# Kernel tuning notes

Measured on AMD Instinct MI355X. Metric: run time of the kernel, lower is better.

## Reference

```python
import jax, jax.numpy as jnp
import numpy as np

B, T, C, L = 512, 512, 96, 64
BLANK = C - 1          # keras ctc_batch_cost uses last class as blank
EPS = 1e-7             # keras.backend.epsilon()
NEG = -1e30            # log-space 'zero'


def setup_inputs() -> dict:
    key = jax.random.key(0)
    k1, k2, k3 = jax.random.split(key, 3)
    # y_pred is expected to be a softmax output (probabilities over classes)
    y_pred = jax.nn.softmax(jax.random.normal(k1, (B, T, C), dtype=jnp.float32), axis=-1)
    # labels exclude the blank class (values in [0, C-2])
    y_true = jax.random.randint(k2, (B, L), 0, C - 1).astype(jnp.int32)
    label_length = jax.random.randint(k3, (B, 1), 16, L + 1).astype(jnp.int32)
    # forward slices y_pred[:, 2:, :] -> effective time length T-2 = 510
    input_length = jnp.full((B, 1), T - 2, dtype=jnp.int32)
    return {"y_true": y_true, "y_pred": y_pred,
            "input_length": input_length, "label_length": label_length}


def _ctc_forward(logprobs, labels, input_len, label_len):
    """CTC negative log-likelihood via the forward (alpha) DP in log space.
    logprobs: [B, Tp, C] log-probabilities; labels: [B, L] int;
    input_len, label_len: [B] int. Returns [B] loss."""
    Bn, Tp, Cn = logprobs.shape
    Ln = labels.shape[1]
    S = 2 * Ln + 1
    s = jnp.arange(S)
    lab_idx = jnp.clip(s // 2, 0, Ln - 1)
    # extended label sequence: blank, l1, blank, l2, ..., blank  -> [B, S]
    ext = jnp.where(s[None, :] % 2 == 1, labels[:, lab_idx], BLANK)
    ext2 = jnp.concatenate([jnp.full((Bn, 2), -1, ext.dtype), ext[:, :-2]], axis=1)
    allow_skip = (ext != BLANK) & (ext != ext2)  # [B, S]

    # gather per-timestep log-probs of extended labels: [Tp, B, S]
    lp_t = jnp.transpose(logprobs, (1, 0, 2))
    lp_ext = jnp.take_along_axis(lp_t, jnp.broadcast_to(ext[None], (Tp, Bn, S)), axis=2)

    # t = 0 init: only s=0 (blank) and s=1 (first label) reachable
    alpha0 = jnp.where(s[None, :] < 2, lp_ext[0], NEG)  # [B, S]

    def step(alpha, xs):
        lp, t = xs
        a1 = jnp.concatenate([jnp.full((Bn, 1), NEG, alpha.dtype), alpha[:, :-1]], axis=1)
        a2 = jnp.concatenate([jnp.full((Bn, 2), NEG, alpha.dtype), alpha[:, :-2]], axis=1)
        a2 = jnp.where(allow_skip, a2, NEG)
        new = jnp.logaddexp(jnp.logaddexp(alpha, a1), a2) + lp
        # freeze alpha once past each sequence's input length
        alpha = jnp.where((t < input_len)[:, None], new, alpha)
        return alpha, None

    ts = jnp.arange(1, Tp)
    alpha, _ = jax.lax.scan(step, alpha0, (lp_ext[1:], ts))

    s_last = 2 * label_len  # index of final blank in extended sequence
    a_last = jnp.take_along_axis(alpha, s_last[:, None], axis=1)[:, 0]
    a_prev = jnp.take_along_axis(alpha, (s_last - 1)[:, None], axis=1)[:, 0]
    return -jnp.logaddexp(a_last, a_prev)


def reference(y_true, y_pred, input_length, label_length):
    # CTCLayer.call: crop first two timesteps, then keras ctc_batch_cost
    y_pred = y_pred[:, 2:, :]
    # keras: logits = log(probs + eps); tf.nn.ctc_loss then log-softmaxes internally
    logits = jnp.log(y_pred + EPS)
    logprobs = jax.nn.log_softmax(logits, axis=-1)
    loss = _ctc_forward(logprobs, y_true,
                        input_length.reshape(-1).astype(jnp.int32),
                        label_length.reshape(-1).astype(jnp.int32))
    return loss[:, None]  # [B, 1], matching ctc_batch_cost's expand_dims
```

## Files before the change

kernel.cpp:

```cpp
#include <hip/hip_runtime.h>


constexpr int   T_    = 512;
constexpr int   C_    = 96;
constexpr int   L_    = 64;
constexpr int   TP_   = 510;
constexpr float EPS_  = 1e-7f;
constexpr float LN2_  = 0.69314718055994530942f;
constexpr float LSE1_ = 1.3849806e-5f;

typedef float f8 __attribute__((ext_vector_type(8)));
typedef float f2 __attribute__((ext_vector_type(2)));

__device__ __forceinline__ float flog2(float x) {
#if __has_builtin(__builtin_amdgcn_logf)
  return __builtin_amdgcn_logf(x);
#else
  return log2f(x);
#endif
}
__device__ __forceinline__ float fexp2(float x) {
#if __has_builtin(__builtin_amdgcn_exp2f)
  return __builtin_amdgcn_exp2f(x);
#else
  return exp2f(x);
#endif
}
__device__ __forceinline__ float fldexp(float x, int n) {
#if __has_builtin(__builtin_amdgcn_ldexpf)
  return __builtin_amdgcn_ldexpf(x, n);
#else
  return __builtin_ldexpf(x, n);
#endif
}

template<int CTRL, int RM, int BM, bool BC>
__device__ __forceinline__ float dppf(float old_, float src) {
  return __int_as_float(__builtin_amdgcn_update_dpp(
      __float_as_int(old_), __float_as_int(src), CTRL, RM, BM, BC));
}
template<int CTRL, int RM, int BM, bool BC>
__device__ __forceinline__ int dppi(int old_, int src) {
  return __builtin_amdgcn_update_dpp(old_, src, CTRL, RM, BM, BC);
}

__device__ __forceinline__ float lae2(float x, float y) {
  float m = fmaxf(x, y);
  return m + flog2(1.f + fexp2(-fabsf(x - y)));
}

#define LOADG(PL, PB, T0) {                                         \
  const float* _bl = colL + (size_t)(T0) * C_;                      \
  const float* _bb = colB + (size_t)(T0) * C_;                      \
  PL.s0=_bl[0*C_]; PB.s0=_bb[0*C_]; PL.s1=_bl[1*C_]; PB.s1=_bb[1*C_];\
  PL.s2=_bl[2*C_]; PB.s2=_bb[2*C_]; PL.s3=_bl[3*C_]; PB.s3=_bb[3*C_];\
  PL.s4=_bl[4*C_]; PB.s4=_bb[4*C_]; PL.s5=_bl[5*C_]; PB.s5=_bb[5*C_];\
  PL.s6=_bl[6*C_]; PB.s6=_bb[6*C_]; PL.s7=_bl[7*C_]; PB.s7=_bb[7*C_]; }

#define LD1C(PL, PB, T0, J) {                                       \
  int _t = (T0) + (J); _t = _t < TP_ ? _t : TP_ - 1;                \
  PL.s##J = colL[(size_t)_t * C_]; PB.s##J = colB[(size_t)_t * C_]; }
#define LOADGC(PL, PB, T0) \
  LD1C(PL,PB,T0,0) LD1C(PL,PB,T0,1) LD1C(PL,PB,T0,2) LD1C(PL,PB,T0,3) \
  LD1C(PL,PB,T0,4) LD1C(PL,PB,T0,5) LD1C(PL,PB,T0,6) LD1C(PL,PB,T0,7)

#define A8(PL, PB) { stepF(PL.s0,PB.s0); stepF(PL.s1,PB.s1);        \
  stepF(PL.s2,PB.s2); stepF(PL.s3,PB.s3); stepF(PL.s4,PB.s4);       \
  stepF(PL.s5,PB.s5); stepF(PL.s6,PB.s6); stepF(PL.s7,PB.s7); }

#define B8(PL, PB) { stepS(PL.s0,PB.s0); stepS(PL.s1,PB.s1);        \
  stepS(PL.s2,PB.s2); stepS(PL.s3,PB.s3); renormS();                \
  stepS(PL.s4,PB.s4); stepS(PL.s5,PB.s5); stepS(PL.s6,PB.s6);       \
  stepS(PL.s7,PB.s7); renormS(); }

#define TAIL1(PL, PB, J, OFF) \
  if ((tb + (OFF) + (J)) < tmax) stepF(PL.s##J, PB.s##J);
#define TAIL8(PL, PB, OFF) \
  TAIL1(PL,PB,0,OFF) TAIL1(PL,PB,1,OFF) TAIL1(PL,PB,2,OFF) TAIL1(PL,PB,3,OFF) \
  TAIL1(PL,PB,4,OFF) TAIL1(PL,PB,5,OFF) TAIL1(PL,PB,6,OFF) TAIL1(PL,PB,7,OFF)

__global__ __launch_bounds__(64, 1) void ctc_fwd(
    const int* __restrict__ y_true, const float* __restrict__ y_pred,
    const int* __restrict__ input_len, const int* __restrict__ label_len,
    float* __restrict__ out)
{
  const int b = blockIdx.x;
  const int l = threadIdx.x;

  const float* __restrict__ rp = y_pred + (size_t)b * T_ * C_ + 2 * C_;
  const int  lab     = y_true[b * L_ + l];
  const int  labPrev = __shfl_up(lab, 1);
  const float skipM  = (l >= 1 && lab != labPrev) ? 1.f : 0.f;
  const int  ilen    = input_len[b];
  const int  llen    = label_len[b];
  const int  tmax    = ilen < TP_ ? ilen : TP_;

  const float* __restrict__ colL = rp + lab;
  const float* __restrict__ colB = rp + (C_ - 1);

  f2    m;
  float mX = 0.f;
  int   e = 0, d = 0;
  m.x = (l == 0) ? (colB[0] + EPS_) : 0.f;
  m.y = (l == 0) ? (colL[0] + EPS_) : 0.f;

  f8 pl0, pl1, pl2, pl3, pb0, pb1, pb2, pb3;
  LOADG(pl0, pb0, 1);  LOADG(pl1, pb1, 9);
  LOADG(pl2, pb2, 17); LOADG(pl3, pb3, 25);

  auto runDP = [&](auto has128) {
    constexpr bool H128 = decltype(has128)::value;

    auto stepF = [&](float pl, float pb) {
      float plE = pl + EPS_, pbE = pb + EPS_;
      int   en  = dppi<0x138, 0xf, 0xf, false>(0, e);
      float m1  = dppf<0x138, 0xf, 0xf, false>(0.f, m.y);
      int   dd  = en - e;  dd = dd < 120 ? dd : 120;
      float a1  = fldexp(m1, dd);
      float nE  = (m.x + a1) * pbE;
      float nO  = fmaf(a1, skipM, m.y + m.x) * plE;
      float nX = 0.f, mx;
      if constexpr (H128) { nX = (mX + m.y) * pbE; mx = fmaxf(fmaxf(nE, nO), nX); }
      else                { mx = fmaxf(nE, nO); }
      int  kb = __float_as_int(mx) >> 23;
      int  ks = 127 - kb;
      bool z  = (mx == 0.f);
      e  = z ? en : (e + kb - 127);
      m.x = fldexp(nE, ks);
      m.y = fldexp(nO, ks);
      if constexpr (H128) mX = fldexp(nX, ks);
    };

    auto stepS = [&](float pl, float pb) {
      f2 p2;  p2.x = pb + EPS_;  p2.y = pl + EPS_;
      float m1 = dppf<0x138, 0xf, 0xf, false>(0.f, m.y);
      float a1 = fldexp(m1, d);
      float t  = fmaf(a1, skipM, m.x);
      if constexpr (H128) mX = (mX + m.y) * p2.x;
      f2 ad;  ad.x = a1;  ad.y = t;
      m = (m + ad) * p2;
    };

    auto renormS = [&]() {
      float mx = fmaxf(m.x, m.y);
      if constexpr (H128) mx = fmaxf(mx, mX);
      int kb = __float_as_int(mx) >> 23;
      int ks = 127 - kb;
      e += kb - 127;
      m.x = fldexp(m.x, ks);
      m.y = fldexp(m.y, ks);
      if constexpr (H128) mX = fldexp(mX, ks);
      int en = dppi<0x138, 0xf, 0xf, false>(0, e);
      int dd = en - e;  d = dd < 120 ? dd : 120;
    };

    int tb = 1;
#pragma unroll 1
    for (; tb < 65 && tb + 64 <= tmax; tb += 32) {
      A8(pl0, pb0); LOADG(pl0, pb0, tb + 32);
      A8(pl1, pb1); LOADG(pl1, pb1, tb + 40);
      A8(pl2, pb2); LOADG(pl2, pb2, tb + 48);
      A8(pl3, pb3); LOADG(pl3, pb3, tb + 56);
    }
    renormS();
#pragma unroll 1
    for (; tb + 64 <= tmax; tb += 32) {
      B8(pl0, pb0); LOADG(pl0, pb0, tb + 32);
      B8(pl1, pb1); LOADG(pl1, pb1, tb + 40);
      B8(pl2, pb2); LOADG(pl2, pb2, tb + 48);
      B8(pl3, pb3); LOADG(pl3, pb3, tb + 56);
    }
#pragma unroll 1
    for (; tb + 32 <= tmax; tb += 32) {
      A8(pl0, pb0); LOADGC(pl0, pb0, tb + 32);
      A8(pl1, pb1); LOADGC(pl1, pb1, tb + 40);
      A8(pl2, pb2); LOADGC(pl2, pb2, tb + 48);
      A8(pl3, pb3); LOADGC(pl3, pb3, tb + 56);
    }
    TAIL8(pl0, pb0, 0); TAIL8(pl1, pb1, 8);
    TAIL8(pl2, pb2, 16); TAIL8(pl3, pb3, 24);
  };

  if (llen >= 64) runDP(std::integral_constant<bool, true>{});
  else            runDP(std::integral_constant<bool, false>{});

  float ef  = (float)e;
  float lgE = flog2(m.x) + ef;
  float lgO = flog2(m.y) + ef;
  float aL;
  if (llen >= 64) { float lgX = flog2(mX) + ef; aL = __shfl(lgX, 63); }
  else            { aL = __shfl(lgE, llen); }
  float aP = __shfl(lgO, llen - 1);
  if (l == 0)
    out[b] = -LN2_ * (lae2(aL, aP) - (float)tmax * LSE1_);
}

extern "C" void kernel_launch(void* const* d_in, const int* in_sizes, int n_in,
                              void* d_out, int out_size, void* d_ws, size_t ws_size,
                              hipStream_t stream) {
  const int*   y_true = (const int*)d_in[0];
  const float* y_pred = (const float*)d_in[1];
  const int*   ilen   = (const int*)d_in[2];
  const int*   llen   = (const int*)d_in[3];
  float*       outp   = (float*)d_out;
  const int    B      = out_size;
  hipLaunchKernelGGL(ctc_fwd, dim3(B), dim3(64), 0, stream,
                     y_true, y_pred, ilen, llen, outp);
}
```

Before: 31.88 us.

## Split CTC kernel into producer wave loading to LDS and consumer DP wave

```diff
diff --git a/kernel.cpp b/kernel.cpp
--- a/kernel.cpp
+++ b/kernel.cpp
@@ -49,43 +49,76 @@
   return m + flog2(1.f + fexp2(-fabsf(x - y)));
 }
 
-#define LOADG(PL, PB, T0) {                                         \
-  const float* _bl = colL + (size_t)(T0) * C_;                      \
-  const float* _bb = colB + (size_t)(T0) * C_;                      \
-  PL.s0=_bl[0*C_]; PB.s0=_bb[0*C_]; PL.s1=_bl[1*C_]; PB.s1=_bb[1*C_];\
-  PL.s2=_bl[2*C_]; PB.s2=_bb[2*C_]; PL.s3=_bl[3*C_]; PB.s3=_bb[3*C_];\
-  PL.s4=_bl[4*C_]; PB.s4=_bb[4*C_]; PL.s5=_bl[5*C_]; PB.s5=_bb[5*C_];\
-  PL.s6=_bl[6*C_]; PB.s6=_bb[6*C_]; PL.s7=_bl[7*C_]; PB.s7=_bb[7*C_]; }
-
-#define LD1C(PL, PB, T0, J) {                                       \
-  int _t = (T0) + (J); _t = _t < TP_ ? _t : TP_ - 1;                \
-  PL.s##J = colL[(size_t)_t * C_]; PB.s##J = colB[(size_t)_t * C_]; }
-#define LOADGC(PL, PB, T0) \
-  LD1C(PL,PB,T0,0) LD1C(PL,PB,T0,1) LD1C(PL,PB,T0,2) LD1C(PL,PB,T0,3) \
-  LD1C(PL,PB,T0,4) LD1C(PL,PB,T0,5) LD1C(PL,PB,T0,6) LD1C(PL,PB,T0,7)
-
-#define A8(PL, PB) { stepF(PL.s0,PB.s0); stepF(PL.s1,PB.s1);        \
-  stepF(PL.s2,PB.s2); stepF(PL.s3,PB.s3); stepF(PL.s4,PB.s4);       \
-  stepF(PL.s5,PB.s5); stepF(PL.s6,PB.s6); stepF(PL.s7,PB.s7); }
-
-#define B8(PL, PB) { stepS(PL.s0,PB.s0); stepS(PL.s1,PB.s1);        \
-  stepS(PL.s2,PB.s2); stepS(PL.s3,PB.s3); renormS();                \
-  stepS(PL.s4,PB.s4); stepS(PL.s5,PB.s5); stepS(PL.s6,PB.s6);       \
-  stepS(PL.s7,PB.s7); renormS(); }
-
-#define TAIL1(PL, PB, J, OFF) \
-  if ((tb + (OFF) + (J)) < tmax) stepF(PL.s##J, PB.s##J);
-#define TAIL8(PL, PB, OFF) \
-  TAIL1(PL,PB,0,OFF) TAIL1(PL,PB,1,OFF) TAIL1(PL,PB,2,OFF) TAIL1(PL,PB,3,OFF) \
-  TAIL1(PL,PB,4,OFF) TAIL1(PL,PB,5,OFF) TAIL1(PL,PB,6,OFF) TAIL1(PL,PB,7,OFF)
-
-__global__ __launch_bounds__(64, 1) void ctc_fwd(
+#define PG8(R, TB) { \
+  R.s0 = gl((TB)+0); R.s1 = gl((TB)+1); R.s2 = gl((TB)+2); R.s3 = gl((TB)+3); \
+  R.s4 = gl((TB)+4); R.s5 = gl((TB)+5); R.s6 = gl((TB)+6); R.s7 = gl((TB)+7); }
+
+#define PLOADB(S, TB) { \
+  PG8(S##0, (TB)+0);  PG8(S##1, (TB)+8);  PG8(S##2, (TB)+16); PG8(S##3, (TB)+24); \
+  PG8(S##4, (TB)+32); PG8(S##5, (TB)+40); PG8(S##6, (TB)+48); PG8(S##7, (TB)+56); \
+  q##S = glb((TB) + l); }
+
+#define PW8(R, PH, TI) { \
+  plb[PH][(TI)+0][l] = R.s0; plb[PH][(TI)+1][l] = R.s1; \
+  plb[PH][(TI)+2][l] = R.s2; plb[PH][(TI)+3][l] = R.s3; \
+  plb[PH][(TI)+4][l] = R.s4; plb[PH][(TI)+5][l] = R.s5; \
+  plb[PH][(TI)+6][l] = R.s6; plb[PH][(TI)+7][l] = R.s7; }
+
+#define PWRITEB(S, PH) { \
+  PW8(S##0, PH, 0)  PW8(S##1, PH, 8)  PW8(S##2, PH, 16) PW8(S##3, PH, 24) \
+  PW8(S##4, PH, 32) PW8(S##5, PH, 40) PW8(S##6, PH, 48) PW8(S##7, PH, 56) \
+  pbb[PH][l] = q##S; }
+
+#define DSR8(PH, J, PL, PB) { \
+  PL.s0 = plb[PH][(J)*8+0][l]; PB.s0 = pbb[PH][(J)*8+0]; \
+  PL.s1 = plb[PH][(J)*8+1][l]; PB.s1 = pbb[PH][(J)*8+1]; \
+  PL.s2 = plb[PH][(J)*8+2][l]; PB.s2 = pbb[PH][(J)*8+2]; \
+  PL.s3 = plb[PH][(J)*8+3][l]; PB.s3 = pbb[PH][(J)*8+3]; \
+  PL.s4 = plb[PH][(J)*8+4][l]; PB.s4 = pbb[PH][(J)*8+4]; \
+  PL.s5 = plb[PH][(J)*8+5][l]; PB.s5 = pbb[PH][(J)*8+5]; \
+  PL.s6 = plb[PH][(J)*8+6][l]; PB.s6 = pbb[PH][(J)*8+6]; \
+  PL.s7 = plb[PH][(J)*8+7][l]; PB.s7 = pbb[PH][(J)*8+7]; }
+
+#define ST8(PL, PB) { renormS(); \
+  stepS(PL.s0,PB.s0); stepS(PL.s1,PB.s1); stepS(PL.s2,PB.s2); stepS(PL.s3,PB.s3); \
+  renormS(); \
+  stepS(PL.s4,PB.s4); stepS(PL.s5,PB.s5); stepS(PL.s6,PB.s6); stepS(PL.s7,PB.s7); }
+
+#define GD8(T0, PL, PB) { \
+  if ((T0)+0 < tmax) stepF(PL.s0,PB.s0); \
+  if ((T0)+1 < tmax) stepF(PL.s1,PB.s1); \
+  if ((T0)+2 < tmax) stepF(PL.s2,PB.s2); \
+  if ((T0)+3 < tmax) stepF(PL.s3,PB.s3); \
+  if ((T0)+4 < tmax) stepF(PL.s4,PB.s4); \
+  if ((T0)+5 < tmax) stepF(PL.s5,PB.s5); \
+  if ((T0)+6 < tmax) stepF(PL.s6,PB.s6); \
+  if ((T0)+7 < tmax) stepF(PL.s7,PB.s7); }
+
+#define COMPG(G, PL, PB) { const int _t0 = 1 + 8*(G); \
+  if ((G) >= 8 && (_t0 + 7) < tmax) ST8(PL, PB) else GD8(_t0, PL, PB) }
+
+#define CONSUME(PH, GB) { \
+  DSR8(PH, 0, plA, pbA); \
+  DSR8(PH, 1, plB, pbB); COMPG((GB)+0, plA, pbA); \
+  DSR8(PH, 2, plA, pbA); COMPG((GB)+1, plB, pbB); \
+  DSR8(PH, 3, plB, pbB); COMPG((GB)+2, plA, pbA); \
+  DSR8(PH, 4, plA, pbA); COMPG((GB)+3, plB, pbB); \
+  DSR8(PH, 5, plB, pbB); COMPG((GB)+4, plA, pbA); \
+  DSR8(PH, 6, plA, pbA); COMPG((GB)+5, plB, pbB); \
+  DSR8(PH, 7, plB, pbB); COMPG((GB)+6, plA, pbA); \
+                         COMPG((GB)+7, plB, pbB); }
+
+__global__ __launch_bounds__(128, 1) void ctc_fwd(
     const int* __restrict__ y_true, const float* __restrict__ y_pred,
     const int* __restrict__ input_len, const int* __restrict__ label_len,
     float* __restrict__ out)
 {
-  const int b = blockIdx.x;
-  const int l = threadIdx.x;
+  __shared__ float plb[2][64][64];
+  __shared__ float pbb[2][64];
+  const int tid = threadIdx.x;
+  const int wid = tid >> 6;
+  const int l   = tid & 63;
+  const int b   = blockIdx.x;
 
   const float* __restrict__ rp = y_pred + (size_t)b * T_ * C_ + 2 * C_;
   const int  lab     = y_true[b * L_ + l];
@@ -98,101 +131,101 @@
   const float* __restrict__ colL = rp + lab;
   const float* __restrict__ colB = rp + (C_ - 1);
 
-  f2    m;
+  auto gl  = [&](int t) -> float { int tc = t < TP_ ? t : TP_ - 1; return colL[(size_t)tc * C_]; };
+  auto glb = [&](int t) -> float { int tc = t < TP_ ? t : TP_ - 1; return colB[(size_t)tc * C_]; };
+
+  f2    mm;
   float mX = 0.f;
   int   e = 0, d = 0;
-  m.x = (l == 0) ? (colB[0] + EPS_) : 0.f;
-  m.y = (l == 0) ? (colL[0] + EPS_) : 0.f;
-
-  f8 pl0, pl1, pl2, pl3, pb0, pb1, pb2, pb3;
-  LOADG(pl0, pb0, 1);  LOADG(pl1, pb1, 9);
-  LOADG(pl2, pb2, 17); LOADG(pl3, pb3, 25);
-
-  auto runDP = [&](auto has128) {
-    constexpr bool H128 = decltype(has128)::value;
+  mm.x = (wid == 0 && l == 0) ? (colB[0] + EPS_) : 0.f;
+  mm.y = (wid == 0 && l == 0) ? (colL[0] + EPS_) : 0.f;
+
+  auto run = [&](auto hasC) {
+    constexpr bool H128 = decltype(hasC)::value;
 
     auto stepF = [&](float pl, float pb) {
       float plE = pl + EPS_, pbE = pb + EPS_;
       int   en  = dppi<0x138, 0xf, 0xf, false>(0, e);
-      float m1  = dppf<0x138, 0xf, 0xf, false>(0.f, m.y);
+      float m1  = dppf<0x138, 0xf, 0xf, false>(0.f, mm.y);
       int   dd  = en - e;  dd = dd < 120 ? dd : 120;
       float a1  = fldexp(m1, dd);
-      float nE  = (m.x + a1) * pbE;
-      float nO  = fmaf(a1, skipM, m.y + m.x) * plE;
+      float nE  = (mm.x + a1) * pbE;
+      float nO  = fmaf(a1, skipM, mm.y + mm.x) * plE;
       float nX = 0.f, mx;
-      if constexpr (H128) { nX = (mX + m.y) * pbE; mx = fmaxf(fmaxf(nE, nO), nX); }
+      if constexpr (H128) { nX = (mX + mm.y) * pbE; mx = fmaxf(fmaxf(nE, nO), nX); }
       else                { mx = fmaxf(nE, nO); }
       int  kb = __float_as_int(mx) >> 23;
       int  ks = 127 - kb;
       bool z  = (mx == 0.f);
       e  = z ? en : (e + kb - 127);
-      m.x = fldexp(nE, ks);
-      m.y = fldexp(nO, ks);
+      mm.x = fldexp(nE, ks);
+      mm.y = fldexp(nO, ks);
       if constexpr (H128) mX = fldexp(nX, ks);
     };
 
     auto stepS = [&](float pl, float pb) {
       f2 p2;  p2.x = pb + EPS_;  p2.y = pl + EPS_;
-      float m1 = dppf<0x138, 0xf, 0xf, false>(0.f, m.y);
+      float m1 = dppf<0x138, 0xf, 0xf, false>(0.f, mm.y);
       float a1 = fldexp(m1, d);
-      float t  = fmaf(a1, skipM, m.x);
-      if constexpr (H128) mX = (mX + m.y) * p2.x;
+      float t  = fmaf(a1, skipM, mm.x);
+      if constexpr (H128) mX = (mX + mm.y) * p2.x;
       f2 ad;  ad.x = a1;  ad.y = t;
-      m = (m + ad) * p2;
+      mm = (mm + ad) * p2;
     };
 
     auto renormS = [&]() {
-      float mx = fmaxf(m.x, m.y);
+      float mx = fmaxf(mm.x, mm.y);
       if constexpr (H128) mx = fmaxf(mx, mX);
       int kb = __float_as_int(mx) >> 23;
       int ks = 127 - kb;
       e += kb - 127;
-      m.x = fldexp(m.x, ks);
-      m.y = fldexp(m.y, ks);
+      mm.x = fldexp(mm.x, ks);
+      mm.y = fldexp(mm.y, ks);
       if constexpr (H128) mX = fldexp(mX, ks);
       int en = dppi<0x138, 0xf, 0xf, false>(0, e);
       int dd = en - e;  d = dd < 120 ? dd : 120;
     };
 
-    int tb = 1;
+    f8 A0,A1,A2,A3,A4,A5,A6,A7, C0,C1,C2,C3,C4,C5,C6,C7;
+    float qA, qC;
+    f8 plA, plB, pbA, pbB;
+
+    if (wid == 1) { PLOADB(A, 1) PLOADB(C, 65) }
+
 #pragma unroll 1
-    for (; tb < 65 && tb + 64 <= tmax; tb += 32) {
-      A8(pl0, pb0); LOADG(pl0, pb0, tb + 32);
-      A8(pl1, pb1); LOADG(pl1, pb1, tb + 40);
-      A8(pl2, pb2); LOADG(pl2, pb2, tb + 48);
-      A8(pl3, pb3); LOADG(pl3, pb3, tb + 56);
+    for (int mp = 0; mp < 8; ++mp) {
+      if (wid == 1) {
+        if (mp & 1) {
+          if (mp < 7) PLOADB(A, 1 + 64 * (mp + 1))
+          PWRITEB(C, 1)
+        } else {
+          if (mp >= 2) PLOADB(C, 1 + 64 * (mp + 1))
+          PWRITEB(A, 0)
+        }
+      } else if (mp >= 1) {
+        const int ph = (mp - 1) & 1;
+        const int gb = (mp - 1) * 8;
+        CONSUME(ph, gb)
+      }
+      __syncthreads();
     }
-    renormS();
-#pragma unroll 1
-    for (; tb + 64 <= tmax; tb += 32) {
-      B8(pl0, pb0); LOADG(pl0, pb0, tb + 32);
-      B8(pl1, pb1); LOADG(pl1, pb1, tb + 40);
-      B8(pl2, pb2); LOADG(pl2, pb2, tb + 48);
-      B8(pl3, pb3); LOADG(pl3, pb3, tb + 56);
-    }
-#pragma unroll 1
-    for (; tb + 32 <= tmax; tb += 32) {
-      A8(pl0, pb0); LOADGC(pl0, pb0, tb + 32);
-      A8(pl1, pb1); LOADGC(pl1, pb1, tb + 40);
-      A8(pl2, pb2); LOADGC(pl2, pb2, tb + 48);
-      A8(pl3, pb3); LOADGC(pl3, pb3, tb + 56);
-    }
-    TAIL8(pl0, pb0, 0); TAIL8(pl1, pb1, 8);
-    TAIL8(pl2, pb2, 16); TAIL8(pl3, pb3, 24);
+    if (wid == 0) CONSUME(1, 56)
   };
 
-  if (llen >= 64) runDP(std::integral_constant<bool, true>{});
-  else            runDP(std::integral_constant<bool, false>{});
-
-  float ef  = (float)e;
-  float lgE = flog2(m.x) + ef;
-  float lgO = flog2(m.y) + ef;
-  float aL;
-  if (llen >= 64) { float lgX = flog2(mX) + ef; aL = __shfl(lgX, 63); }
-  else            { aL = __shfl(lgE, llen); }
-  float aP = __shfl(lgO, llen - 1);
-  if (l == 0)
-    out[b] = -LN2_ * (lae2(aL, aP) - (float)tmax * LSE1_);
+  if (llen >= 64) run(std::integral_constant<bool, true>{});
+  else            run(std::integral_constant<bool, false>{});
+
+  if (wid == 0) {
+    float ef  = (float)e;
+    float lgE = flog2(mm.x) + ef;
+    float lgO = flog2(mm.y) + ef;
+    float aL;
+    if (llen >= 64) { float lgX = flog2(mX) + ef; aL = __shfl(lgX, 63); }
+    else            { aL = __shfl(lgE, llen); }
+    float aP = __shfl(lgO, llen - 1);
+    if (l == 0)
+      out[b] = -LN2_ * (lae2(aL, aP) - (float)tmax * LSE1_);
+  }
 }
 
 extern "C" void kernel_launch(void* const* d_in, const int* in_sizes, int n_in,
@@ -204,6 +237,6 @@
   const int*   llen   = (const int*)d_in[3];
   float*       outp   = (float*)d_out;
   const int    B      = out_size;
-  hipLaunchKernelGGL(ctc_fwd, dim3(B), dim3(64), 0, stream,
+  hipLaunchKernelGGL(ctc_fwd, dim3(B), dim3(128), 0, stream,
                      y_true, y_pred, ilen, llen, outp);
 }
```

Result: slower. 35.27 us (+10.6%).

## Fuse two CTC time steps per cross-lane exchange in the scaled DP

Applied to the files above, without the earlier changes.

```diff
diff --git a/kernel.cpp b/kernel.cpp
--- a/kernel.cpp
+++ b/kernel.cpp
@@ -49,35 +49,98 @@
   return m + flog2(1.f + fexp2(-fabsf(x - y)));
 }
 
-#define LOADG(PL, PB, T0) {                                         \
-  const float* _bl = colL + (size_t)(T0) * C_;                      \
-  const float* _bb = colB + (size_t)(T0) * C_;                      \
-  PL.s0=_bl[0*C_]; PB.s0=_bb[0*C_]; PL.s1=_bl[1*C_]; PB.s1=_bb[1*C_];\
-  PL.s2=_bl[2*C_]; PB.s2=_bb[2*C_]; PL.s3=_bl[3*C_]; PB.s3=_bb[3*C_];\
-  PL.s4=_bl[4*C_]; PB.s4=_bb[4*C_]; PL.s5=_bl[5*C_]; PB.s5=_bb[5*C_];\
-  PL.s6=_bl[6*C_]; PB.s6=_bb[6*C_]; PL.s7=_bl[7*C_]; PB.s7=_bb[7*C_]; }
-
-#define LD1C(PL, PB, T0, J) {                                       \
-  int _t = (T0) + (J); _t = _t < TP_ ? _t : TP_ - 1;                \
-  PL.s##J = colL[(size_t)_t * C_]; PB.s##J = colB[(size_t)_t * C_]; }
-#define LOADGC(PL, PB, T0) \
-  LD1C(PL,PB,T0,0) LD1C(PL,PB,T0,1) LD1C(PL,PB,T0,2) LD1C(PL,PB,T0,3) \
-  LD1C(PL,PB,T0,4) LD1C(PL,PB,T0,5) LD1C(PL,PB,T0,6) LD1C(PL,PB,T0,7)
-
-#define A8(PL, PB) { stepF(PL.s0,PB.s0); stepF(PL.s1,PB.s1);        \
-  stepF(PL.s2,PB.s2); stepF(PL.s3,PB.s3); stepF(PL.s4,PB.s4);       \
-  stepF(PL.s5,PB.s5); stepF(PL.s6,PB.s6); stepF(PL.s7,PB.s7); }
-
-#define B8(PL, PB) { stepS(PL.s0,PB.s0); stepS(PL.s1,PB.s1);        \
-  stepS(PL.s2,PB.s2); stepS(PL.s3,PB.s3); renormS();                \
-  stepS(PL.s4,PB.s4); stepS(PL.s5,PB.s5); stepS(PL.s6,PB.s6);       \
-  stepS(PL.s7,PB.s7); renormS(); }
-
-#define TAIL1(PL, PB, J, OFF) \
-  if ((tb + (OFF) + (J)) < tmax) stepF(PL.s##J, PB.s##J);
-#define TAIL8(PL, PB, OFF) \
-  TAIL1(PL,PB,0,OFF) TAIL1(PL,PB,1,OFF) TAIL1(PL,PB,2,OFF) TAIL1(PL,PB,3,OFF) \
-  TAIL1(PL,PB,4,OFF) TAIL1(PL,PB,5,OFF) TAIL1(PL,PB,6,OFF) TAIL1(PL,PB,7,OFF)
+#define LOADF8(R, BASE, T0) { const float* _p = (BASE) + (size_t)(T0) * C_;  \
+  R .s0=_p[0];    R .s1=_p[C_];   R .s2=_p[2*C_]; R .s3=_p[3*C_];            \
+  R .s4=_p[4*C_]; R .s5=_p[5*C_]; R .s6=_p[6*C_]; R .s7=_p[7*C_]; }
+
+#define LOADPP(R, T0) { const float* _p = colP + (size_t)(T0) * C_;          \
+  R .s0=_p[0];     R .s1=_p[2*C_];  R .s2=_p[4*C_];  R .s3=_p[6*C_];         \
+  R .s4=_p[8*C_];  R .s5=_p[10*C_]; R .s6=_p[12*C_]; R .s7=_p[14*C_]; }
+
+#define LD1C(R, BASE, T0, J) { int _t = (T0) + (J);                          \
+  _t = _t < TP_ ? _t : TP_ - 1; R .s##J = (BASE)[(size_t)_t * C_]; }
+#define LOADF8C(R, BASE, T0)                                                 \
+  LD1C(R,BASE,T0,0) LD1C(R,BASE,T0,1) LD1C(R,BASE,T0,2) LD1C(R,BASE,T0,3)    \
+  LD1C(R,BASE,T0,4) LD1C(R,BASE,T0,5) LD1C(R,BASE,T0,6) LD1C(R,BASE,T0,7)
+#define LP1C(R, T0, J) { int _t = (T0) + 2*(J);                              \
+  _t = _t < TP_ ? _t : TP_ - 1; R .s##J = colP[(size_t)_t * C_]; }
+#define LOADPPC(R, T0)                                                       \
+  LP1C(R,T0,0) LP1C(R,T0,1) LP1C(R,T0,2) LP1C(R,T0,3)                        \
+  LP1C(R,T0,4) LP1C(R,T0,5) LP1C(R,T0,6) LP1C(R,T0,7)
+
+#define REFILL_H1(BK, T0) { LOADF8(PL##BK##0, colL, T0)                      \
+                            LOADF8(PB##BK##0, colB, T0) }
+#define REFILL_H2(BK, T0) { LOADF8(PL##BK##1, colL, (T0)+8)                  \
+                            LOADF8(PB##BK##1, colB, (T0)+8)                  \
+                            LOADPP(PP##BK, T0) }
+#define REFILLC(BK, T0)   { LOADF8C(PL##BK##0, colL, T0)                     \
+                            LOADF8C(PB##BK##0, colB, T0)                     \
+                            LOADF8C(PL##BK##1, colL, (T0)+8)                 \
+                            LOADF8C(PB##BK##1, colB, (T0)+8) }
+
+#define FPAIR(PL1V, PB1V, PL2V, PB2V, PPV) {                                 \
+  float pb1E = (PB1V) + EPS_, pl1E = (PL1V) + EPS_;                          \
+  float pb2E = (PB2V) + EPS_, pl2E = (PL2V) + EPS_;                          \
+  float ppE  = (PPV) + EPS_;                                                 \
+  float mO1s = dppf<0x138, 0xf, 0xf, false>(0.f, mm.y);        \
+  float mE1s = dppf<0x138, 0xf, 0xf, false>(0.f, mm.x);        \
+  float mO2s = dppf<0x138, 0xf, 0xf, false>(0.f, mO1s);        \
+  float aO   = fldexp(mO1s, d);                                              \
+  float aE   = fldexp(mE1s, d);                                              \
+  float aO2  = fldexp(mO2s, d2);                                             \
+  float E1   = (mm.x + aO) * pb1E;                                           \
+  float O1   = fmaf(aO, skipM, mm.y + mm.x) * pl1E;                          \
+  float O1n  = fmaf(aO2, skipP, aO + aE) * ppE;                              \
+  if constexpr (H128) { float X1 = (mX + mm.y) * pb1E;                       \
+                        mX = (X1 + O1) * pb2E; }                             \
+  float E2   = (E1 + O1n) * pb2E;                                            \
+  float O2   = fmaf(O1n, skipM, O1 + E1) * pl2E;                             \
+  mm.x = E2; mm.y = O2; }
+
+#define FSB(BK, TNXT) {                                                      \
+  FPAIR(PL##BK##0 .s0, PB##BK##0 .s0, PL##BK##0 .s1, PB##BK##0 .s1, PP##BK .s0) \
+  FPAIR(PL##BK##0 .s2, PB##BK##0 .s2, PL##BK##0 .s3, PB##BK##0 .s3, PP##BK .s1) \
+  renormS();                                                                 \
+  FPAIR(PL##BK##0 .s4, PB##BK##0 .s4, PL##BK##0 .s5, PB##BK##0 .s5, PP##BK .s2) \
+  FPAIR(PL##BK##0 .s6, PB##BK##0 .s6, PL##BK##0 .s7, PB##BK##0 .s7, PP##BK .s3) \
+  renormS();                                                                 \
+  REFILL_H1(BK, TNXT)                                                        \
+  FPAIR(PL##BK##1 .s0, PB##BK##1 .s0, PL##BK##1 .s1, PB##BK##1 .s1, PP##BK .s4) \
+  FPAIR(PL##BK##1 .s2, PB##BK##1 .s2, PL##BK##1 .s3, PB##BK##1 .s3, PP##BK .s5) \
+  renormS();                                                                 \
+  FPAIR(PL##BK##1 .s4, PB##BK##1 .s4, PL##BK##1 .s5, PB##BK##1 .s5, PP##BK .s6) \
+  FPAIR(PL##BK##1 .s6, PB##BK##1 .s6, PL##BK##1 .s7, PB##BK##1 .s7, PP##BK .s7) \
+  renormS();                                                                 \
+  REFILL_H2(BK, TNXT) }
+
+#define FILLSB(BK, TNXT) {                                                   \
+  stepF(PL##BK##0 .s0, PB##BK##0 .s0); stepF(PL##BK##0 .s1, PB##BK##0 .s1);  \
+  stepF(PL##BK##0 .s2, PB##BK##0 .s2); stepF(PL##BK##0 .s3, PB##BK##0 .s3);  \
+  stepF(PL##BK##0 .s4, PB##BK##0 .s4); stepF(PL##BK##0 .s5, PB##BK##0 .s5);  \
+  stepF(PL##BK##0 .s6, PB##BK##0 .s6); stepF(PL##BK##0 .s7, PB##BK##0 .s7);  \
+  REFILL_H1(BK, TNXT)                                                        \
+  stepF(PL##BK##1 .s0, PB##BK##1 .s0); stepF(PL##BK##1 .s1, PB##BK##1 .s1);  \
+  stepF(PL##BK##1 .s2, PB##BK##1 .s2); stepF(PL##BK##1 .s3, PB##BK##1 .s3);  \
+  stepF(PL##BK##1 .s4, PB##BK##1 .s4); stepF(PL##BK##1 .s5, PB##BK##1 .s5);  \
+  stepF(PL##BK##1 .s6, PB##BK##1 .s6); stepF(PL##BK##1 .s7, PB##BK##1 .s7);  \
+  REFILL_H2(BK, TNXT) }
+
+#define G1(BK, HF, T0, J)                                                    \
+  if ((T0) + (J) < tmax) stepF(PL##BK##HF .s##J, PB##BK##HF .s##J);
+#define GUARD16(BK, T0) {                                                    \
+  G1(BK,0,T0,0) G1(BK,0,T0,1) G1(BK,0,T0,2) G1(BK,0,T0,3)                    \
+  G1(BK,0,T0,4) G1(BK,0,T0,5) G1(BK,0,T0,6) G1(BK,0,T0,7)                    \
+  { const int _u0 = (T0) + 8;                                                \
+    G1(BK,1,_u0,0) G1(BK,1,_u0,1) G1(BK,1,_u0,2) G1(BK,1,_u0,3)              \
+    G1(BK,1,_u0,4) G1(BK,1,_u0,5) G1(BK,1,_u0,6) G1(BK,1,_u0,7) } }
+
+#define TAILX(B1, B2) {                                                      \
+  GUARD16(B1, tb)                                                            \
+  REFILLC(B1, tb + 32)                                                       \
+  GUARD16(B2, tb + 16)                                                       \
+  REFILLC(B2, tb + 48)                                                       \
+  GUARD16(B1, tb + 32)                                                       \
+  GUARD16(B2, tb + 48) }
 
 __global__ __launch_bounds__(64, 1) void ctc_fwd(
     const int* __restrict__ y_true, const float* __restrict__ y_pred,
@@ -91,102 +154,94 @@
   const int  lab     = y_true[b * L_ + l];
   const int  labPrev = __shfl_up(lab, 1);
   const float skipM  = (l >= 1 && lab != labPrev) ? 1.f : 0.f;
+  const float skipP  = __shfl_up(skipM, 1);
   const int  ilen    = input_len[b];
   const int  llen    = label_len[b];
   const int  tmax    = ilen < TP_ ? ilen : TP_;
 
   const float* __restrict__ colL = rp + lab;
+  const float* __restrict__ colP = rp + labPrev;
   const float* __restrict__ colB = rp + (C_ - 1);
 
-  f2    m;
+  f2    mm;
   float mX = 0.f;
-  int   e = 0, d = 0;
-  m.x = (l == 0) ? (colB[0] + EPS_) : 0.f;
-  m.y = (l == 0) ? (colL[0] + EPS_) : 0.f;
-
-  f8 pl0, pl1, pl2, pl3, pb0, pb1, pb2, pb3;
-  LOADG(pl0, pb0, 1);  LOADG(pl1, pb1, 9);
-  LOADG(pl2, pb2, 17); LOADG(pl3, pb3, 25);
-
-  auto runDP = [&](auto has128) {
-    constexpr bool H128 = decltype(has128)::value;
+  int   e = 0, d = 0, d2 = 0;
+  mm.x = (l == 0) ? (colB[0] + EPS_) : 0.f;
+  mm.y = (l == 0) ? (colL[0] + EPS_) : 0.f;
+
+  f8 PLa0, PLa1, PBa0, PBa1, PPa, PLb0, PLb1, PBb0, PBb1, PPb;
+  LOADF8C(PLa0, colL, 1)  LOADF8C(PBa0, colB, 1)
+  LOADF8C(PLa1, colL, 9)  LOADF8C(PBa1, colB, 9)   LOADPPC(PPa, 1)
+  LOADF8C(PLb0, colL, 17) LOADF8C(PBb0, colB, 17)
+  LOADF8C(PLb1, colL, 25) LOADF8C(PBb1, colB, 25)  LOADPPC(PPb, 17)
+
+  auto runDP = [&](auto hasC) {
+    constexpr bool H128 = decltype(hasC)::value;
 
     auto stepF = [&](float pl, float pb) {
       float plE = pl + EPS_, pbE = pb + EPS_;
       int   en  = dppi<0x138, 0xf, 0xf, false>(0, e);
-      float m1  = dppf<0x138, 0xf, 0xf, false>(0.f, m.y);
+      float m1  = dppf<0x138, 0xf, 0xf, false>(0.f, mm.y);
       int   dd  = en - e;  dd = dd < 120 ? dd : 120;
       float a1  = fldexp(m1, dd);
-      float nE  = (m.x + a1) * pbE;
-      float nO  = fmaf(a1, skipM, m.y + m.x) * plE;
+      float nE  = (mm.x + a1) * pbE;
+      float nO  = fmaf(a1, skipM, mm.y + mm.x) * plE;
       float nX = 0.f, mx;
-      if constexpr (H128) { nX = (mX + m.y) * pbE; mx = fmaxf(fmaxf(nE, nO), nX); }
+      if constexpr (H128) { nX = (mX + mm.y) * pbE; mx = fmaxf(fmaxf(nE, nO), nX); }
       else                { mx = fmaxf(nE, nO); }
       int  kb = __float_as_int(mx) >> 23;
       int  ks = 127 - kb;
       bool z  = (mx == 0.f);
       e  = z ? en : (e + kb - 127);
-      m.x = fldexp(nE, ks);
-      m.y = fldexp(nO, ks);
+      mm.x = fldexp(nE, ks);
+      mm.y = fldexp(nO, ks);
       if constexpr (H128) mX = fldexp(nX, ks);
     };
 
-    auto stepS = [&](float pl, float pb) {
-      f2 p2;  p2.x = pb + EPS_;  p2.y = pl + EPS_;
-      float m1 = dppf<0x138, 0xf, 0xf, false>(0.f, m.y);
-      float a1 = fldexp(m1, d);
-      float t  = fmaf(a1, skipM, m.x);
-      if constexpr (H128) mX = (mX + m.y) * p2.x;
-      f2 ad;  ad.x = a1;  ad.y = t;
-      m = (m + ad) * p2;
-    };
-
     auto renormS = [&]() {
-      float mx = fmaxf(m.x, m.y);
+      float mx = fmaxf(mm.x, mm.y);
       if constexpr (H128) mx = fmaxf(mx, mX);
       int kb = __float_as_int(mx) >> 23;
       int ks = 127 - kb;
       e += kb - 127;
-      m.x = fldexp(m.x, ks);
-      m.y = fldexp(m.y, ks);
+      mm.x = fldexp(mm.x, ks);
+      mm.y = fldexp(mm.y, ks);
       if constexpr (H128) mX = fldexp(mX, ks);
-      int en = dppi<0x138, 0xf, 0xf, false>(0, e);
-      int dd = en - e;  d = dd < 120 ? dd : 120;
+      int en  = dppi<0x138, 0xf, 0xf, false>(0, e);
+      int en2 = dppi<0x138, 0xf, 0xf, false>(0, en);
+      int dd  = en  - e;  d  = dd  < 120 ? dd  : 120;
+      int dd2 = en2 - e;  d2 = dd2 < 120 ? dd2 : 120;
     };
 
     int tb = 1;
+    if (tmax >= 81) {
+      FILLSB(a, 33) FILLSB(b, 49) FILLSB(a, 65) FILLSB(b, 81)
+      tb = 65;
+      renormS();
 #pragma unroll 1
-    for (; tb < 65 && tb + 64 <= tmax; tb += 32) {
-      A8(pl0, pb0); LOADG(pl0, pb0, tb + 32);
-      A8(pl1, pb1); LOADG(pl1, pb1, tb + 40);
-      A8(pl2, pb2); LOADG(pl2, pb2, tb + 48);
-      A8(pl3, pb3); LOADG(pl3, pb3, tb + 56);
+      for (; tb + 64 <= tmax; ) {
+        FSB(a, tb + 32) tb += 16;
+        FSB(b, tb + 32) tb += 16;
+      }
+      if (tb + 48 <= tmax) {
+        FSB(a, tb + 32) tb += 16;
+        TAILX(b, a)
+      } else {
+        TAILX(a, b)
+      }
+    } else {
+#pragma unroll 1
+      for (int t = 1; t < tmax; ++t)
+        stepF(colL[(size_t)t * C_], colB[(size_t)t * C_]);
     }
-    renormS();
-#pragma unroll 1
-    for (; tb + 64 <= tmax; tb += 32) {
-      B8(pl0, pb0); LOADG(pl0, pb0, tb + 32);
-      B8(pl1, pb1); LOADG(pl1, pb1, tb + 40);
-      B8(pl2, pb2); LOADG(pl2, pb2, tb + 48);
-      B8(pl3, pb3); LOADG(pl3, pb3, tb + 56);
-    }
-#pragma unroll 1
-    for (; tb + 32 <= tmax; tb += 32) {
-      A8(pl0, pb0); LOADGC(pl0, pb0, tb + 32);
-      A8(pl1, pb1); LOADGC(pl1, pb1, tb + 40);
-      A8(pl2, pb2); LOADGC(pl2, pb2, tb + 48);
-      A8(pl3, pb3); LOADGC(pl3, pb3, tb + 56);
-    }
-    TAIL8(pl0, pb0, 0); TAIL8(pl1, pb1, 8);
-    TAIL8(pl2, pb2, 16); TAIL8(pl3, pb3, 24);
   };
 
   if (llen >= 64) runDP(std::integral_constant<bool, true>{});
   else            runDP(std::integral_constant<bool, false>{});
 
   float ef  = (float)e;
-  float lgE = flog2(m.x) + ef;
-  float lgO = flog2(m.y) + ef;
+  float lgE = flog2(mm.x) + ef;
+  float lgO = flog2(mm.y) + ef;
   float aL;
   if (llen >= 64) { float lgX = flog2(mX) + ef; aL = __shfl(lgX, 63); }
   else            { aL = __shfl(lgE, llen); }
```

Result: slower. 39.97 us (+25.4%).

## Skew CTC alpha recursion across lanes to take cross-lane exchange off critical path

Applied to the files above, without the earlier changes.

```diff
diff --git a/kernel.cpp b/kernel.cpp
--- a/kernel.cpp
+++ b/kernel.cpp
@@ -49,35 +49,35 @@
   return m + flog2(1.f + fexp2(-fabsf(x - y)));
 }
 
-#define LOADG(PL, PB, T0) {                                         \
-  const float* _bl = colL + (size_t)(T0) * C_;                      \
-  const float* _bb = colB + (size_t)(T0) * C_;                      \
-  PL.s0=_bl[0*C_]; PB.s0=_bb[0*C_]; PL.s1=_bl[1*C_]; PB.s1=_bb[1*C_];\
-  PL.s2=_bl[2*C_]; PB.s2=_bb[2*C_]; PL.s3=_bl[3*C_]; PB.s3=_bb[3*C_];\
-  PL.s4=_bl[4*C_]; PB.s4=_bb[4*C_]; PL.s5=_bl[5*C_]; PB.s5=_bb[5*C_];\
-  PL.s6=_bl[6*C_]; PB.s6=_bb[6*C_]; PL.s7=_bl[7*C_]; PB.s7=_bb[7*C_]; }
-
-#define LD1C(PL, PB, T0, J) {                                       \
-  int _t = (T0) + (J); _t = _t < TP_ ? _t : TP_ - 1;                \
-  PL.s##J = colL[(size_t)_t * C_]; PB.s##J = colB[(size_t)_t * C_]; }
-#define LOADGC(PL, PB, T0) \
-  LD1C(PL,PB,T0,0) LD1C(PL,PB,T0,1) LD1C(PL,PB,T0,2) LD1C(PL,PB,T0,3) \
-  LD1C(PL,PB,T0,4) LD1C(PL,PB,T0,5) LD1C(PL,PB,T0,6) LD1C(PL,PB,T0,7)
-
-#define A8(PL, PB) { stepF(PL.s0,PB.s0); stepF(PL.s1,PB.s1);        \
-  stepF(PL.s2,PB.s2); stepF(PL.s3,PB.s3); stepF(PL.s4,PB.s4);       \
-  stepF(PL.s5,PB.s5); stepF(PL.s6,PB.s6); stepF(PL.s7,PB.s7); }
-
-#define B8(PL, PB) { stepS(PL.s0,PB.s0); stepS(PL.s1,PB.s1);        \
-  stepS(PL.s2,PB.s2); stepS(PL.s3,PB.s3); renormS();                \
-  stepS(PL.s4,PB.s4); stepS(PL.s5,PB.s5); stepS(PL.s6,PB.s6);       \
-  stepS(PL.s7,PB.s7); renormS(); }
-
-#define TAIL1(PL, PB, J, OFF) \
-  if ((tb + (OFF) + (J)) < tmax) stepF(PL.s##J, PB.s##J);
-#define TAIL8(PL, PB, OFF) \
-  TAIL1(PL,PB,0,OFF) TAIL1(PL,PB,1,OFF) TAIL1(PL,PB,2,OFF) TAIL1(PL,PB,3,OFF) \
-  TAIL1(PL,PB,4,OFF) TAIL1(PL,PB,5,OFF) TAIL1(PL,PB,6,OFF) TAIL1(PL,PB,7,OFF)
+#define LOADU8(R, BASE, I0) {                                            \
+  const float* _p = (BASE) + (ptrdiff_t)((I0) - l) * C_;                 \
+  R .s0=_p[0];    R .s1=_p[C_];   R .s2=_p[2*C_]; R .s3=_p[3*C_];        \
+  R .s4=_p[4*C_]; R .s5=_p[5*C_]; R .s6=_p[6*C_]; R .s7=_p[7*C_]; }
+#define REFU(BK, I0) { LOADU8(PL##BK, colL, I0) LOADU8(PB##BK, colB, I0) }
+
+#define LDC1(R, BASE, I0, J) { int _t = (I0) + (J) - l;                  \
+  _t = _t < 1 ? 1 : _t;  _t = _t > TP_ - 1 ? TP_ - 1 : _t;               \
+  R .s##J = (BASE)[(size_t)_t * C_]; }
+#define LOADC8(R, BASE, I0)                                              \
+  LDC1(R,BASE,I0,0) LDC1(R,BASE,I0,1) LDC1(R,BASE,I0,2) LDC1(R,BASE,I0,3)\
+  LDC1(R,BASE,I0,4) LDC1(R,BASE,I0,5) LDC1(R,BASE,I0,6) LDC1(R,BASE,I0,7)
+#define REFC(BK, I0) { LOADC8(PL##BK, colL, I0) LOADC8(PB##BK, colB, I0) }
+
+#define SS8(BK) {                                                        \
+  stepS(PL##BK .s0, PB##BK .s0); stepS(PL##BK .s1, PB##BK .s1);          \
+  stepS(PL##BK .s2, PB##BK .s2); stepS(PL##BK .s3, PB##BK .s3);          \
+  renormS();                                                             \
+  stepS(PL##BK .s4, PB##BK .s4); stepS(PL##BK .s5, PB##BK .s5);          \
+  stepS(PL##BK .s6, PB##BK .s6); stepS(PL##BK .s7, PB##BK .s7);          \
+  renormS(); }
+
+#define SG8(BK, IB) {                                                    \
+  stepG(PL##BK .s0, PB##BK .s0, (IB)+0); stepG(PL##BK .s1, PB##BK .s1, (IB)+1); \
+  stepG(PL##BK .s2, PB##BK .s2, (IB)+2); stepG(PL##BK .s3, PB##BK .s3, (IB)+3); \
+  renormS();                                                             \
+  stepG(PL##BK .s4, PB##BK .s4, (IB)+4); stepG(PL##BK .s5, PB##BK .s5, (IB)+5); \
+  stepG(PL##BK .s6, PB##BK .s6, (IB)+6); stepG(PL##BK .s7, PB##BK .s7, (IB)+7); \
+  renormS(); }
 
 __global__ __launch_bounds__(64, 1) void ctc_fwd(
     const int* __restrict__ y_true, const float* __restrict__ y_pred,
@@ -94,99 +94,121 @@
   const int  ilen    = input_len[b];
   const int  llen    = label_len[b];
   const int  tmax    = ilen < TP_ ? ilen : TP_;
+  const int  tmaxM1  = tmax - 1;
 
   const float* __restrict__ colL = rp + lab;
   const float* __restrict__ colB = rp + (C_ - 1);
 
-  f2    m;
+  f2    mm;
   float mX = 0.f;
+  float q0 = 0.f;
   int   e = 0, d = 0;
-  m.x = (l == 0) ? (colB[0] + EPS_) : 0.f;
-  m.y = (l == 0) ? (colL[0] + EPS_) : 0.f;
-
-  f8 pl0, pl1, pl2, pl3, pb0, pb1, pb2, pb3;
-  LOADG(pl0, pb0, 1);  LOADG(pl1, pb1, 9);
-  LOADG(pl2, pb2, 17); LOADG(pl3, pb3, 25);
-
-  auto runDP = [&](auto has128) {
-    constexpr bool H128 = decltype(has128)::value;
+  mm.x = (l == 0) ? (colB[0] + EPS_) : 0.f;
+  mm.y = (l == 0) ? (colL[0] + EPS_) : 0.f;
+
+  f8 PLa, PBa, PLb, PBb, PLc, PBc, PLd, PBd;
+
+  auto runDP = [&](auto hasC) {
+    constexpr bool H128 = decltype(hasC)::value;
+
+    auto stepS = [&](float pl, float pb) {
+      float tmp = dppf<0x138, 0xf, 0xf, false>(0.f, mm.y);
+      float pbE = pb + EPS_, plE = pl + EPS_;
+      float nE  = (mm.x + q0) * pbE;
+      float s   = mm.x + mm.y;
+      float nO  = fmaf(q0, skipM, s) * plE;
+      if constexpr (H128) mX = (mX + mm.y) * pbE;
+      mm.x = nE; mm.y = nO;
+      q0 = fldexp(tmp, d);
+    };
+
+    auto stepG = [&](float pl, float pb, int iv) {
+      float tmp = dppf<0x138, 0xf, 0xf, false>(0.f, mm.y);
+      float pbE = pb + EPS_, plE = pl + EPS_;
+      float nE  = (mm.x + q0) * pbE;
+      float s   = mm.x + mm.y;
+      float nO  = fmaf(q0, skipM, s) * plE;
+      int   u   = iv - l;
+      bool  act = (u >= 1) && (u <= tmaxM1);
+      if constexpr (H128) { float nX = (mX + mm.y) * pbE; mX = act ? nX : mX; }
+      mm.x = act ? nE : mm.x;
+      mm.y = act ? nO : mm.y;
+      q0 = fldexp(tmp, d);
+    };
+
+    auto renormS = [&]() {
+      float mx = fmaxf(mm.x, mm.y);
+      if constexpr (H128) mx = fmaxf(mx, mX);
+      int  kb = __float_as_int(mx) >> 23;
+      bool z  = (mx == 0.f);
+      int  en = dppi<0x138, 0xf, 0xf, false>(0, e);
+      int  ks = z ? 0 : (127 - kb);
+      e = z ? en : (e + kb - 127);
+      mm.x = fldexp(mm.x, ks);
+      mm.y = fldexp(mm.y, ks);
+      if constexpr (H128) mX = fldexp(mX, ks);
+      q0 = fldexp(q0, ks);
+      int en2 = dppi<0x138, 0xf, 0xf, false>(0, e);
+      int dd  = en2 - e;  d = dd < 120 ? dd : 120;
+    };
 
     auto stepF = [&](float pl, float pb) {
       float plE = pl + EPS_, pbE = pb + EPS_;
       int   en  = dppi<0x138, 0xf, 0xf, false>(0, e);
-      float m1  = dppf<0x138, 0xf, 0xf, false>(0.f, m.y);
+      float m1  = dppf<0x138, 0xf, 0xf, false>(0.f, mm.y);
       int   dd  = en - e;  dd = dd < 120 ? dd : 120;
       float a1  = fldexp(m1, dd);
-      float nE  = (m.x + a1) * pbE;
-      float nO  = fmaf(a1, skipM, m.y + m.x) * plE;
+      float nE  = (mm.x + a1) * pbE;
+      float nO  = fmaf(a1, skipM, mm.y + mm.x) * plE;
       float nX = 0.f, mx;
-      if constexpr (H128) { nX = (mX + m.y) * pbE; mx = fmaxf(fmaxf(nE, nO), nX); }
+      if constexpr (H128) { nX = (mX + mm.y) * pbE; mx = fmaxf(fmaxf(nE, nO), nX); }
       else                { mx = fmaxf(nE, nO); }
       int  kb = __float_as_int(mx) >> 23;
       int  ks = 127 - kb;
       bool z  = (mx == 0.f);
       e  = z ? en : (e + kb - 127);
-      m.x = fldexp(nE, ks);
-      m.y = fldexp(nO, ks);
+      mm.x = fldexp(nE, ks);
+      mm.y = fldexp(nO, ks);
       if constexpr (H128) mX = fldexp(nX, ks);
     };
 
-    auto stepS = [&](float pl, float pb) {
-      f2 p2;  p2.x = pb + EPS_;  p2.y = pl + EPS_;
-      float m1 = dppf<0x138, 0xf, 0xf, false>(0.f, m.y);
-      float a1 = fldexp(m1, d);
-      float t  = fmaf(a1, skipM, m.x);
-      if constexpr (H128) mX = (mX + m.y) * p2.x;
-      f2 ad;  ad.x = a1;  ad.y = t;
-      m = (m + ad) * p2;
-    };
-
-    auto renormS = [&]() {
-      float mx = fmaxf(m.x, m.y);
-      if constexpr (H128) mx = fmaxf(mx, mX);
-      int kb = __float_as_int(mx) >> 23;
-      int ks = 127 - kb;
-      e += kb - 127;
-      m.x = fldexp(m.x, ks);
-      m.y = fldexp(m.y, ks);
-      if constexpr (H128) mX = fldexp(mX, ks);
-      int en = dppi<0x138, 0xf, 0xf, false>(0, e);
-      int dd = en - e;  d = dd < 120 ? dd : 120;
-    };
-
-    int tb = 1;
-#pragma unroll 1
-    for (; tb < 65 && tb + 64 <= tmax; tb += 32) {
-      A8(pl0, pb0); LOADG(pl0, pb0, tb + 32);
-      A8(pl1, pb1); LOADG(pl1, pb1, tb + 40);
-      A8(pl2, pb2); LOADG(pl2, pb2, tb + 48);
-      A8(pl3, pb3); LOADG(pl3, pb3, tb + 56);
+    if (tmax >= 128) {
+      REFC(a, 1) REFC(b, 9) REFC(c, 17) REFC(d, 25)
+      int ib = 1;
+#pragma unroll 1
+      for (int k = 0; k < 2; ++k) {
+        SG8(a, ib) REFC(a, ib + 32) ib += 8;
+        SG8(b, ib) REFC(b, ib + 32) ib += 8;
+        SG8(c, ib) REFC(c, ib + 32) ib += 8;
+        SG8(d, ib) REFC(d, ib + 32) ib += 8;
+      }
+#pragma unroll 1
+      for (; ib + 64 <= tmax; ib += 32) {
+        SS8(a) REFU(a, ib + 32)
+        SS8(b) REFU(b, ib + 40)
+        SS8(c) REFU(c, ib + 48)
+        SS8(d) REFU(d, ib + 56)
+      }
+#pragma unroll 1
+      for (int k = 0; k < 4; ++k) {
+        SG8(a, ib) REFC(a, ib + 32) ib += 8;
+        SG8(b, ib) REFC(b, ib + 32) ib += 8;
+        SG8(c, ib) REFC(c, ib + 32) ib += 8;
+        SG8(d, ib) REFC(d, ib + 32) ib += 8;
+      }
+    } else {
+#pragma unroll 1
+      for (int t = 1; t < tmax; ++t)
+        stepF(colL[(size_t)t * C_], colB[(size_t)t * C_]);
     }
-    renormS();
-#pragma unroll 1
-    for (; tb + 64 <= tmax; tb += 32) {
-      B8(pl0, pb0); LOADG(pl0, pb0, tb + 32);
-      B8(pl1, pb1); LOADG(pl1, pb1, tb + 40);
-      B8(pl2, pb2); LOADG(pl2, pb2, tb + 48);
-      B8(pl3, pb3); LOADG(pl3, pb3, tb + 56);
-    }
-#pragma unroll 1
-    for (; tb + 32 <= tmax; tb += 32) {
-      A8(pl0, pb0); LOADGC(pl0, pb0, tb + 32);
-      A8(pl1, pb1); LOADGC(pl1, pb1, tb + 40);
-      A8(pl2, pb2); LOADGC(pl2, pb2, tb + 48);
-      A8(pl3, pb3); LOADGC(pl3, pb3, tb + 56);
-    }
-    TAIL8(pl0, pb0, 0); TAIL8(pl1, pb1, 8);
-    TAIL8(pl2, pb2, 16); TAIL8(pl3, pb3, 24);
   };
 
   if (llen >= 64) runDP(std::integral_constant<bool, true>{});
   else            runDP(std::integral_constant<bool, false>{});
 
   float ef  = (float)e;
-  float lgE = flog2(m.x) + ef;
-  float lgO = flog2(m.y) + ef;
+  float lgE = flog2(mm.x) + ef;
+  float lgO = flog2(mm.y) + ef;
   float aL;
   if (llen >= 64) { float lgX = flog2(mX) + ef; aL = __shfl(lgX, 63); }
   else            { aL = __shfl(lgE, llen); }
```

New measurement: 66.80 us. +109.5%, slower.
